# Optimization experiments

Hardware: AMD Instinct MI355X
Metric: run time of the kernel (lower is better)

Reference implementation:

```python
import jax, jax.numpy as jnp
import numpy as np

N_NODES = 50000
N_EDGES = 1600000
IN_DIM = 128
HID = 64
EPS = 1e-6


def setup_inputs() -> dict:
    key = jax.random.key(0)
    ks = jax.random.split(key, 12)
    def g(k, shape, scale):
        return jax.random.normal(k, shape, dtype=jnp.float32) * scale
    x = g(ks[0], (N_NODES, IN_DIM), 1.0)
    edge_index = jax.random.randint(ks[1], (2, N_EDGES), 0, N_NODES, dtype=jnp.int64)
    return {
        "x": x,
        "edge_index": edge_index,
        "w0s": g(ks[2], (IN_DIM, HID), 1.0 / np.sqrt(IN_DIM)),
        "w0n": g(ks[3], (IN_DIM, HID), 1.0 / np.sqrt(IN_DIM)),
        "w1s": g(ks[4], (HID, HID), 1.0 / np.sqrt(HID)),
        "w1n": g(ks[5], (HID, HID), 1.0 / np.sqrt(HID)),
        "w2s": g(ks[6], (HID, HID), 1.0 / np.sqrt(HID)),
        "w2n": g(ks[7], (HID, HID), 1.0 / np.sqrt(HID)),
        "mw1": g(ks[8], (HID, 32), 1.0 / np.sqrt(HID)),
        "mb1": jnp.zeros((32,), jnp.float32),
        "mw2": g(ks[9], (32, 1), 1.0 / np.sqrt(32.0)),
        "mb2": jnp.zeros((1,), jnp.float32),
    }


def _uhg_layer(h, src, dst, inv_deg, ws, wn):
    # transform-then-gather (cheaper: GEMM at node granularity, gather at edge granularity)
    msg = (h @ wn)[src]                                    # [E, HID]
    agg = jax.ops.segment_sum(msg, dst, num_segments=N_NODES) * inv_deg  # mean over in-neighbors
    h2 = jax.nn.relu(h @ ws + agg)
    # projective (UHG) normalization: map embedding back onto the unit sphere / projective rep
    return h2 / (jnp.linalg.norm(h2, axis=-1, keepdims=True) + EPS)


def reference(x, edge_index, w0s, w0n, w1s, w1n, w2s, w2n, mw1, mb1, mw2, mb2):
    src, dst = edge_index[0], edge_index[1]
    deg = jax.ops.segment_sum(jnp.ones((N_EDGES,), jnp.float32), dst, num_segments=N_NODES)
    inv_deg = (1.0 / jnp.maximum(deg, 1.0))[:, None]       # [N,1]
    h = _uhg_layer(x, src, dst, inv_deg, w0s, w0n)
    h = _uhg_layer(h, src, dst, inv_deg, w1s, w1n)
    h = _uhg_layer(h, src, dst, inv_deg, w2s, w2n)
    h = jax.nn.relu(h @ mw1 + mb1)                         # [N,32]
    return jax.nn.sigmoid(h @ mw2 + mb2)                   # [N,1]
```

## Files before the change

kernel.cpp:

```cpp
#include <hip/hip_runtime.h>
#include <hip/hip_bf16.h>
#include <math.h>

#define N_NODES 50000
#define N_EDGES 1600000
#define IN_DIM  128
#define HID     64
#define EPB     4096
#define NBLK    391
#define NB      391
#define CAP     8192
static constexpr float EPS = 1e-6f;

typedef __attribute__((ext_vector_type(8))) short          short8;
typedef __attribute__((ext_vector_type(8))) unsigned short ushort8;
typedef __attribute__((ext_vector_type(4))) unsigned short bf16x4_t;
typedef __attribute__((ext_vector_type(4))) int            i32x4;
typedef __attribute__((ext_vector_type(4))) float          f32x4;
typedef __attribute__((ext_vector_type(2))) float          f32x2;

__device__ __forceinline__ float bf2f(unsigned int hi_bits) {
    union { unsigned int i; float f; } c; c.i = hi_bits; return c.f;
}
__device__ __forceinline__ unsigned short f2bf(float f) {
    union { float f; unsigned int i; } c; c.f = f;
    unsigned int r = c.i + 0x7FFFu + ((c.i >> 16) & 1u);
    return (unsigned short)(r >> 16);
}
__device__ __forceinline__ unsigned char f2fp8(float f) {
    int p = __builtin_amdgcn_cvt_pk_fp8_f32(f, f, 0, false);
    return (unsigned char)(p & 0xff);
}


template <int K>
__device__ __forceinline__ void pack_body(const float* __restrict__ wS,
                                          const float* __restrict__ wN,
                                          unsigned short* __restrict__ pS,
                                          unsigned short* __restrict__ pN, int blk) {
    constexpr int NSLOT = (K / 32) * 4 * 64;
    int slot = blk * 256 + (int)threadIdx.x;
    if (slot >= NSLOT) return;
    int lane = slot & 63;
    int ct   = slot >> 6;
    int t    = ct & 3;
    int c    = ct >> 2;
    int m    = lane & 15;
    int quad = lane >> 4;
    int col  = t * 16 + m;
#pragma unroll
    for (int j = 0; j < 8; ++j) {
        int k = c * 32 + quad * 8 + j;
        pS[slot * 8 + j] = f2bf(wS[k * 64 + col]);
        pN[slot * 8 + j] = f2bf(wN[k * 64 + col]);
    }
}


__global__ __launch_bounds__(256) void bucket_count_pack(
    const int* __restrict__ ei, int* __restrict__ blockCounts,
    const float* __restrict__ w0s, const float* __restrict__ w0n,
    const float* __restrict__ w1s, const float* __restrict__ w1n,
    const float* __restrict__ w2s, const float* __restrict__ w2n,
    unsigned short* __restrict__ p0S, unsigned short* __restrict__ p0N,
    unsigned short* __restrict__ p1S, unsigned short* __restrict__ p1N,
    unsigned short* __restrict__ p2S, unsigned short* __restrict__ p2N,
    unsigned char* __restrict__ hnq) {
    if (blockIdx.x >= NBLK) {
        int blk = blockIdx.x - NBLK;
        if (blk == 7 && threadIdx.x >= 128 && threadIdx.x < 144)
            ((unsigned int*)(hnq + (size_t)N_NODES * HID))[threadIdx.x - 128] = 0u;
        if (blk < 4)      pack_body<IN_DIM>(w0s, w0n, p0S, p0N, blk);
        else if (blk < 6) pack_body<HID>(w1s, w1n, p1S, p1N, blk - 4);
        else              pack_body<HID>(w2s, w2n, p2S, p2N, blk - 6);
        return;
    }
    __shared__ int hist[NB];
    for (int i = threadIdx.x; i < NB; i += 256) hist[i] = 0;
    __syncthreads();
    int base = blockIdx.x * EPB;
    int lim  = min(EPB, N_EDGES - base);
    for (int i = threadIdx.x; i < lim; i += 256)
        atomicAdd(&hist[ei[N_EDGES + base + i] >> 7], 1);
    __syncthreads();
    for (int b = threadIdx.x; b < NB; b += 256)
        blockCounts[blockIdx.x * NB + b] = hist[b];
}

template <int K, bool F32IN>
__device__ __forceinline__ void gemm_body(
    const void* __restrict__ Av,
    const unsigned short* __restrict__ pS,
    const unsigned short* __restrict__ pN,
    float* __restrict__ hs, unsigned char* __restrict__ hnq, int blk) {
    constexpr int NC = K / 32;
    int lane = threadIdx.x & 63;
    int wv   = threadIdx.x >> 6;
    int tile = blk * 4 + wv;
    if (tile >= N_NODES / 16) return;
    int m    = lane & 15;
    int quad = lane >> 4;

    const short8* pSf = (const short8*)pS;
    const short8* pNf = (const short8*)pN;

    f32x4 accS[4], accN[4];
#pragma unroll
    for (int t = 0; t < 4; ++t) {
        accS[t] = (f32x4){0.f, 0.f, 0.f, 0.f};
        accN[t] = (f32x4){0.f, 0.f, 0.f, 0.f};
    }
#pragma unroll
    for (int c = 0; c < NC; ++c) {
        short8 a;
        if constexpr (F32IN) {
            const float* Af = (const float*)Av + ((size_t)tile * 16 + m) * K + quad * 8 + c * 32;
            f32x4 a0 = *(const f32x4*)Af;
            f32x4 a1 = *(const f32x4*)(Af + 4);
#pragma unroll
            for (int k = 0; k < 4; ++k) a[k]     = (short)f2bf(a0[k]);
#pragma unroll
            for (int k = 0; k < 4; ++k) a[k + 4] = (short)f2bf(a1[k]);
        } else {
            const short8* Af = (const short8*)((const unsigned short*)Av +
                               ((size_t)tile * 16 + m) * K + quad * 8);
            a = Af[c * 4];
        }
#pragma unroll
        for (int t = 0; t < 4; ++t) {
            short8 bs = pSf[(c * 4 + t) * 64 + lane];
            short8 bn = pNf[(c * 4 + t) * 64 + lane];
            accS[t] = __builtin_amdgcn_mfma_f32_16x16x32_bf16(a, bs, accS[t], 0, 0, 0);
            accN[t] = __builtin_amdgcn_mfma_f32_16x16x32_bf16(a, bn, accN[t], 0, 0, 0);
        }
    }
    int row0 = tile * 16 + quad * 4;
#pragma unroll
    for (int t = 0; t < 4; ++t) {
#pragma unroll
        for (int r = 0; r < 4; ++r) {
            size_t o = (size_t)(row0 + r) * HID + t * 16 + m;
            hs[o]  = accS[t][r];
            hnq[o] = f2fp8(accN[t][r]);
        }
    }
}

__global__ __launch_bounds__(256) void col_sum_gemm0(
    const int* __restrict__ blockCounts, int* __restrict__ totals,
    const float* __restrict__ x,
    const unsigned short* __restrict__ p0S, const unsigned short* __restrict__ p0N,
    float* __restrict__ hs, unsigned char* __restrict__ hnq) {
    if (blockIdx.x >= NB) {
        gemm_body<IN_DIM, true>(x, p0S, p0N, hs, hnq, blockIdx.x - NB);
        return;
    }
    __shared__ int ws[4];
    int b = blockIdx.x;
    int s = 0;
    for (int i = threadIdx.x; i < NBLK; i += 256) s += blockCounts[i * NB + b];
#pragma unroll
    for (int off = 32; off >= 1; off >>= 1) s += __shfl_xor(s, off, 64);
    if ((threadIdx.x & 63) == 0) ws[threadIdx.x >> 6] = s;
    __syncthreads();
    if (threadIdx.x == 0) totals[b] = ws[0] + ws[1] + ws[2] + ws[3];
}

__global__ __launch_bounds__(256) void col_fix_base(int* __restrict__ blockCounts,
                                                    const int* __restrict__ totals,
                                                    int* __restrict__ bucketBase) {
    __shared__ int vals[NBLK];
    __shared__ int sbase;
    int b = blockIdx.x;
    for (int i = threadIdx.x; i < NBLK; i += 256) vals[i] = blockCounts[i * NB + b];
    if (threadIdx.x < 64) {
        int lane = threadIdx.x;
        int s = 0;
        for (int i = lane; i < b; i += 64) s += totals[i];
#pragma unroll
        for (int off = 32; off >= 1; off >>= 1) s += __shfl_xor(s, off, 64);
        if (lane == 0) {
            sbase = s;
            bucketBase[b] = s;
            if (b == NB - 1) bucketBase[NB] = s + totals[b];
        }
    }
    __syncthreads();
    if (threadIdx.x < 64) {
        int lane  = threadIdx.x;
        int carry = sbase;
        for (int base = 0; base < NBLK; base += 64) {
            int i = base + lane;
            int v = (i < NBLK) ? vals[i] : 0;
            int incl = v;
#pragma unroll
            for (int off = 1; off < 64; off <<= 1) {
                int t = __shfl_up(incl, off, 64);
                if (lane >= off) incl += t;
            }
            if (i < NBLK) vals[i] = carry + incl - v;
            carry += __shfl(incl, 63, 64);
        }
    }
    __syncthreads();
    for (int i = threadIdx.x; i < NBLK; i += 256) blockCounts[i * NB + b] = vals[i];
}

__global__ __launch_bounds__(256) void bucket_scatter(const int* __restrict__ ei,
                                                      const int* __restrict__ blockCounts,
                                                      unsigned int* __restrict__ bucketPacked) {
    __shared__ int cur[NB];
    for (int b = threadIdx.x; b < NB; b += 256)
        cur[b] = blockCounts[blockIdx.x * NB + b];
    __syncthreads();
    int base = blockIdx.x * EPB;
    int lim  = min(EPB, N_EDGES - base);
    for (int i = threadIdx.x; i < lim; i += 256) {
        int s = ei[base + i];
        int d = ei[N_EDGES + base + i];
        int pos = atomicAdd(&cur[d >> 7], 1);
        bucketPacked[pos] = ((unsigned int)s << 7) | (unsigned int)(d & 127);
    }
}

__global__ __launch_bounds__(256) void node_scan_scatter(
    const unsigned int* __restrict__ bucketPacked, const int* __restrict__ bucketBase,
    int* __restrict__ rowptr, int* __restrict__ csr_src) {
    __shared__ int cnt[128];
    __shared__ int half0;
    __shared__ unsigned int stage[CAP];
    int tid = threadIdx.x;
    if (tid < 128) cnt[tid] = 0;
    __syncthreads();
    int beg = bucketBase[blockIdx.x], end = bucketBase[blockIdx.x + 1];
    int n = end - beg;
    for (int i = tid; i < n; i += 256) {
        unsigned int e = bucketPacked[beg + i];
        if (i < CAP) stage[i] = e;
        atomicAdd(&cnt[e & 127], 1);
    }
    __syncthreads();
    int lane = tid & 63;
    int v    = (tid < 128) ? cnt[tid] : 0;
    int incl = v;
#pragma unroll
    for (int off = 1; off < 64; off <<= 1) {
        int t = __shfl_up(incl, off, 64);
        if (lane >= off) incl += t;
    }
    if (tid == 63) half0 = incl;
    __syncthreads();
    int base  = beg + ((tid >= 64 && tid < 128) ? half0 : 0);
    int start = base + incl - v;
    int node  = blockIdx.x * 128 + tid;
    if (tid < 128) {
        if (node < N_NODES) rowptr[node] = start;
        cnt[tid] = start;
    }
    if (blockIdx.x == 0 && tid == 128) rowptr[N_NODES] = N_EDGES;
    __syncthreads();
    for (int i = tid; i < n; i += 256) {
        unsigned int e = (i < CAP) ? stage[i] : bucketPacked[beg + i];
        int pos = atomicAdd(&cnt[e & 127], 1);
        csr_src[pos] = (int)(e >> 7);
    }
}

template <int K, bool F32IN>
__global__ __launch_bounds__(256) void gemm_dual_mfma(
    const void* __restrict__ Av,
    const unsigned short* __restrict__ pS,
    const unsigned short* __restrict__ pN,
    float* __restrict__ hs, unsigned char* __restrict__ hnq) {
    gemm_body<K, F32IN>(Av, pS, pN, hs, hnq, blockIdx.x);
}

template <bool MLP>
__global__ __launch_bounds__(256) void agg_update(
    const int* __restrict__ rowptr, const int* __restrict__ csr_src,
    const unsigned char* __restrict__ hnq, const float* __restrict__ hs,
    unsigned short* __restrict__ hb_out,
    const float* __restrict__ mw1, const float* __restrict__ mb1,
    const float* __restrict__ mw2, const float* __restrict__ mb2,
    float* __restrict__ out) {
    __shared__ float sW1[MLP ? HID * 32 : 1];
    __shared__ float sW2[MLP ? 32 : 1];
    __shared__ float sB1[MLP ? 32 : 1];
    __shared__ float sH[MLP ? 16 * 68 : 1];
    if (MLP) {
        for (int i = threadIdx.x; i < HID * 32; i += 256) sW1[i] = mw1[i];
        if (threadIdx.x < 32) { sW2[threadIdx.x] = mw2[threadIdx.x]; sB1[threadIdx.x] = mb1[threadIdx.x]; }
        __syncthreads();
    }
    int sn   = threadIdx.x >> 4;
    int r    = threadIdx.x & 15;
    int node = blockIdx.x * 16 + sn;
    int beg = rowptr[node];
    int end = rowptr[node + 1];
    int deg = end - beg;
    int tbase = beg & ~7;
    int nbat  = (end - tbase + 7) >> 3;
    const i32x4* ip = (const i32x4*)(csr_src + tbase);
    const unsigned char* hrow = hnq + r * 4;

    f32x2 acc2[2];
    acc2[0] = (f32x2){0.f, 0.f};
    acc2[1] = (f32x2){0.f, 0.f};
    int pr = tbase - beg;

#pragma unroll 2
    for (int t = 0; t < nbat; ++t) {
        i32x4 a = ip[2 * t];
        i32x4 b = ip[2 * t + 1];
        int p0 = pr + 8 * t;
        int si[8];
#pragma unroll
        for (int u = 0; u < 4; ++u) {
            si[u]     = ((unsigned)(p0 + u)     < (unsigned)deg) ? a[u] : N_NODES;
            si[u + 4] = ((unsigned)(p0 + 4 + u) < (unsigned)deg) ? b[u] : N_NODES;
        }
        unsigned wv[8];
#pragma unroll
        for (int u = 0; u < 8; ++u)
            wv[u] = *(const unsigned*)(hrow + ((unsigned)si[u] << 6));
#pragma unroll
        for (int u = 0; u < 8; ++u) {
#if __has_builtin(__builtin_amdgcn_cvt_pk_f32_fp8)
            acc2[0] += __builtin_amdgcn_cvt_pk_f32_fp8((int)wv[u], false);
            acc2[1] += __builtin_amdgcn_cvt_pk_f32_fp8((int)wv[u], true);
#else
            acc2[0] += (f32x2){__builtin_amdgcn_cvt_f32_fp8((int)wv[u], 0),
                               __builtin_amdgcn_cvt_f32_fp8((int)wv[u], 1)};
            acc2[1] += (f32x2){__builtin_amdgcn_cvt_f32_fp8((int)wv[u], 2),
                               __builtin_amdgcn_cvt_f32_fp8((int)wv[u], 3)};
#endif
        }
    }

    float acc[4] = {acc2[0][0], acc2[0][1], acc2[1][0], acc2[1][1]};
    float invdeg = 1.0f / fmaxf((float)deg, 1.0f);
    f32x4 h = *(const f32x4*)(hs + (size_t)node * HID + r * 4);
    float v[4], ss = 0.f;
#pragma unroll
    for (int k = 0; k < 4; ++k) {
        v[k] = fmaxf(fmaf(acc[k], invdeg, h[k]), 0.f);
        ss += v[k] * v[k];
    }
    ss += __shfl_xor(ss, 1, 64);
    ss += __shfl_xor(ss, 2, 64);
    ss += __shfl_xor(ss, 4, 64);
    ss += __shfl_xor(ss, 8, 64);
    float rs = 1.0f / (sqrtf(ss) + EPS);
    if (MLP) {
#pragma unroll
        for (int k = 0; k < 4; ++k) sH[sn * 68 + r * 4 + k] = v[k] * rs;
        __syncthreads();
        int c0 = r * 2;
        float y0 = sB1[c0], y1 = sB1[c0 + 1];
        const float* hrow2 = &sH[sn * 68];
#pragma unroll 8
        for (int k = 0; k < HID; ++k) {
            float hv = hrow2[k];
            y0 = fmaf(hv, sW1[k * 32 + c0], y0);
            y1 = fmaf(hv, sW1[k * 32 + c0 + 1], y1);
        }
        float p = fmaxf(y0, 0.f) * sW2[c0] + fmaxf(y1, 0.f) * sW2[c0 + 1];
        p += __shfl_xor(p, 1, 64);
        p += __shfl_xor(p, 2, 64);
        p += __shfl_xor(p, 4, 64);
        p += __shfl_xor(p, 8, 64);
        if (r == 0) out[node] = 1.0f / (1.0f + __expf(-(p + mb2[0])));
    } else {
        bf16x4_t o;
#pragma unroll
        for (int k = 0; k < 4; ++k) o[k] = f2bf(v[k] * rs);
        *(bf16x4_t*)(hb_out + (size_t)node * HID + r * 4) = o;
    }
}

extern "C" void kernel_launch(void* const* d_in, const int* in_sizes, int n_in,
                              void* d_out, int out_size, void* d_ws, size_t ws_size,
                              hipStream_t stream) {
    const float* x   = (const float*)d_in[0];
    const int*   ei  = (const int*)d_in[1];
    const float* w0s = (const float*)d_in[2];
    const float* w0n = (const float*)d_in[3];
    const float* w1s = (const float*)d_in[4];
    const float* w1n = (const float*)d_in[5];
    const float* w2s = (const float*)d_in[6];
    const float* w2n = (const float*)d_in[7];
    const float* mw1 = (const float*)d_in[8];
    const float* mb1 = (const float*)d_in[9];
    const float* mw2 = (const float*)d_in[10];
    const float* mb2 = (const float*)d_in[11];
    float*       out = (float*)d_out;

    int* rowptr      = (int*)d_ws;
    int* csr_src     = rowptr + 50432;
    int* blockCounts = csr_src + N_EDGES;
    int* bucketBase  = blockCounts + 153600;
    int* totals      = bucketBase + 512;
    unsigned int* bucketPacked = (unsigned int*)(totals + 512);
    const size_t NH = (size_t)N_NODES * HID;
    float*          hs  = (float*)(bucketPacked + N_EDGES);
    unsigned char*  hnq = (unsigned char*)(hs + NH);
    unsigned short* hb  = (unsigned short*)(hnq + NH + 64);
    unsigned short* p0S = hb + NH;
    unsigned short* p0N = p0S + IN_DIM * HID;
    unsigned short* p1S = p0N + IN_DIM * HID;
    unsigned short* p1N = p1S + HID * HID;
    unsigned short* p2S = p1N + HID * HID;
    unsigned short* p2N = p2S + HID * HID;

    const int nodeGrid = N_NODES / 16;
    const int gemmGrid = (N_NODES / 16 + 3) / 4;

    bucket_count_pack<<<NBLK + 8, 256, 0, stream>>>(
        ei, blockCounts, w0s, w0n, w1s, w1n, w2s, w2n,
        p0S, p0N, p1S, p1N, p2S, p2N, hnq);
    col_sum_gemm0<<<NB + gemmGrid, 256, 0, stream>>>(
        blockCounts, totals, x, p0S, p0N, hs, hnq);
    col_fix_base<<<NB, 256, 0, stream>>>(blockCounts, totals, bucketBase);
    bucket_scatter<<<NBLK, 256, 0, stream>>>(ei, blockCounts, bucketPacked);
    node_scan_scatter<<<NB, 256, 0, stream>>>(bucketPacked, bucketBase, rowptr, csr_src);

    agg_update<false><<<nodeGrid, 256, 0, stream>>>(
        rowptr, csr_src, hnq, hs, hb, nullptr, nullptr, nullptr, nullptr, nullptr);

    gemm_dual_mfma<HID, false><<<gemmGrid, 256, 0, stream>>>(hb, p1S, p1N, hs, hnq);
    agg_update<false><<<nodeGrid, 256, 0, stream>>>(
        rowptr, csr_src, hnq, hs, hb, nullptr, nullptr, nullptr, nullptr, nullptr);

    gemm_dual_mfma<HID, false><<<gemmGrid, 256, 0, stream>>>(hb, p2S, p2N, hs, hnq);
    agg_update<true><<<nodeGrid, 256, 0, stream>>>(
        rowptr, csr_src, hnq, hs, nullptr, mw1, mb1, mw2, mb2, out);
}
```

Before: 223.6 us.

## Fuse next-layer GEMM into aggregation and pad CSR rows to multiples of eight

Each non-final aggregation kernel now stages its normalized 16-node tile in shared memory as bf16 and runs the next layer's dual MFMA GEMM directly, writing the fp32 self term and fp8 neighbor term into ping-pong buffers. This removes the two standalone GEMM launches and the bf16 hidden-state round trip through global memory. The CSR is also rebuilt with per-node padding to multiples of eight using a dummy node index, so the gather loop can drop its per-edge bounds masking. The cost is a larger padded CSR buffer, per-bucket capacity assumptions (8192 slots), and an extra block barrier plus MFMA work inside the latency-bound gather kernel.

```diff
diff --git a/kernel.cpp b/kernel.cpp
--- a/kernel.cpp
+++ b/kernel.cpp
@@ -10,6 +10,7 @@
 #define NBLK    391
 #define NB      391
 #define CAP     8192
+#define PBKT    8192
 static constexpr float EPS = 1e-6f;
 
 typedef __attribute__((ext_vector_type(8))) short          short8;
@@ -19,9 +20,6 @@
 typedef __attribute__((ext_vector_type(4))) float          f32x4;
 typedef __attribute__((ext_vector_type(2))) float          f32x2;
 
-__device__ __forceinline__ float bf2f(unsigned int hi_bits) {
-    union { unsigned int i; float f; } c; c.i = hi_bits; return c.f;
-}
 __device__ __forceinline__ unsigned short f2bf(float f) {
     union { float f; unsigned int i; } c; c.f = f;
     unsigned int r = c.i + 0x7FFFu + ((c.i >> 16) & 1u);
@@ -65,11 +63,15 @@
     unsigned short* __restrict__ p0S, unsigned short* __restrict__ p0N,
     unsigned short* __restrict__ p1S, unsigned short* __restrict__ p1N,
     unsigned short* __restrict__ p2S, unsigned short* __restrict__ p2N,
-    unsigned char* __restrict__ hnq) {
+    unsigned char* __restrict__ hnqA, unsigned char* __restrict__ hnqB) {
     if (blockIdx.x >= NBLK) {
         int blk = blockIdx.x - NBLK;
-        if (blk == 7 && threadIdx.x >= 128 && threadIdx.x < 144)
-            ((unsigned int*)(hnq + (size_t)N_NODES * HID))[threadIdx.x - 128] = 0u;
+        if (blk == 7) {
+            if (threadIdx.x >= 128 && threadIdx.x < 144)
+                ((unsigned int*)(hnqA + (size_t)N_NODES * HID))[threadIdx.x - 128] = 0u;
+            if (threadIdx.x >= 144 && threadIdx.x < 160)
+                ((unsigned int*)(hnqB + (size_t)N_NODES * HID))[threadIdx.x - 144] = 0u;
+        }
         if (blk < 4)      pack_body<IN_DIM>(w0s, w0n, p0S, p0N, blk);
         else if (blk < 6) pack_body<HID>(w1s, w1n, p1S, p1N, blk - 4);
         else              pack_body<HID>(w2s, w2n, p2S, p2N, blk - 6);
@@ -223,9 +225,9 @@
     }
 }
 
-__global__ __launch_bounds__(256) void node_scan_scatter(
+__global__ __launch_bounds__(256) void node_scan_scatter_pad(
     const unsigned int* __restrict__ bucketPacked, const int* __restrict__ bucketBase,
-    int* __restrict__ rowptr, int* __restrict__ csr_src) {
+    int* __restrict__ pbeg, int* __restrict__ rdeg, int* __restrict__ csr_pad) {
     __shared__ int cnt[128];
     __shared__ int half0;
     __shared__ unsigned int stage[CAP];
@@ -242,7 +244,8 @@
     __syncthreads();
     int lane = tid & 63;
     int v    = (tid < 128) ? cnt[tid] : 0;
-    int incl = v;
+    int vp   = (v + 7) & ~7;
+    int incl = vp;
 #pragma unroll
     for (int off = 1; off < 64; off <<= 1) {
         int t = __shfl_up(incl, off, 64);
@@ -250,39 +253,33 @@
     }
     if (tid == 63) half0 = incl;
     __syncthreads();
-    int base  = beg + ((tid >= 64 && tid < 128) ? half0 : 0);
-    int start = base + incl - v;
+    int start = blockIdx.x * PBKT + ((tid >= 64 && tid < 128) ? half0 : 0) + incl - vp;
     int node  = blockIdx.x * 128 + tid;
-    if (tid < 128) {
-        if (node < N_NODES) rowptr[node] = start;
+    if (tid < 128 && node < N_NODES) {
+        pbeg[node] = start;
+        rdeg[node] = v;
+        for (int j = v; j < vp; ++j) csr_pad[start + j] = N_NODES;
         cnt[tid] = start;
     }
-    if (blockIdx.x == 0 && tid == 128) rowptr[N_NODES] = N_EDGES;
     __syncthreads();
     for (int i = tid; i < n; i += 256) {
         unsigned int e = (i < CAP) ? stage[i] : bucketPacked[beg + i];
         int pos = atomicAdd(&cnt[e & 127], 1);
-        csr_src[pos] = (int)(e >> 7);
-    }
-}
-
-template <int K, bool F32IN>
-__global__ __launch_bounds__(256) void gemm_dual_mfma(
-    const void* __restrict__ Av,
-    const unsigned short* __restrict__ pS,
-    const unsigned short* __restrict__ pN,
-    float* __restrict__ hs, unsigned char* __restrict__ hnq) {
-    gemm_body<K, F32IN>(Av, pS, pN, hs, hnq, blockIdx.x);
+        csr_pad[pos] = (int)(e >> 7);
+    }
 }
 
 template <bool MLP>
 __global__ __launch_bounds__(256) void agg_update(
-    const int* __restrict__ rowptr, const int* __restrict__ csr_src,
+    const int* __restrict__ pbeg, const int* __restrict__ rdeg,
+    const int* __restrict__ csr_pad,
     const unsigned char* __restrict__ hnq, const float* __restrict__ hs,
-    unsigned short* __restrict__ hb_out,
+    const unsigned short* __restrict__ pS, const unsigned short* __restrict__ pN,
+    float* __restrict__ hs2, unsigned char* __restrict__ hnq2,
     const float* __restrict__ mw1, const float* __restrict__ mb1,
     const float* __restrict__ mw2, const float* __restrict__ mb2,
     float* __restrict__ out) {
+    __shared__ unsigned short sA[MLP ? 1 : 16 * 80];
     __shared__ float sW1[MLP ? HID * 32 : 1];
     __shared__ float sW2[MLP ? 32 : 1];
     __shared__ float sB1[MLP ? 32 : 1];
@@ -295,34 +292,27 @@
     int sn   = threadIdx.x >> 4;
     int r    = threadIdx.x & 15;
     int node = blockIdx.x * 16 + sn;
-    int beg = rowptr[node];
-    int end = rowptr[node + 1];
-    int deg = end - beg;
-    int tbase = beg & ~7;
-    int nbat  = (end - tbase + 7) >> 3;
-    const i32x4* ip = (const i32x4*)(csr_src + tbase);
-    const unsigned char* hrow = hnq + r * 4;
+    int beg  = pbeg[node];
+    int dg   = rdeg[node];
+    int nbat = (dg + 7) >> 3;
+    const i32x4* ip = (const i32x4*)(csr_pad + beg);
+    unsigned r4 = (unsigned)(r * 4);
 
     f32x2 acc2[2];
     acc2[0] = (f32x2){0.f, 0.f};
     acc2[1] = (f32x2){0.f, 0.f};
-    int pr = tbase - beg;
 
 #pragma unroll 2
     for (int t = 0; t < nbat; ++t) {
         i32x4 a = ip[2 * t];
         i32x4 b = ip[2 * t + 1];
-        int p0 = pr + 8 * t;
-        int si[8];
-#pragma unroll
-        for (int u = 0; u < 4; ++u) {
-            si[u]     = ((unsigned)(p0 + u)     < (unsigned)deg) ? a[u] : N_NODES;
-            si[u + 4] = ((unsigned)(p0 + 4 + u) < (unsigned)deg) ? b[u] : N_NODES;
-        }
         unsigned wv[8];
 #pragma unroll
-        for (int u = 0; u < 8; ++u)
-            wv[u] = *(const unsigned*)(hrow + ((unsigned)si[u] << 6));
+        for (int u = 0; u < 4; ++u)
+            wv[u]     = *(const unsigned*)(hnq + (((unsigned)a[u] << 6) + r4));
+#pragma unroll
+        for (int u = 0; u < 4; ++u)
+            wv[u + 4] = *(const unsigned*)(hnq + (((unsigned)b[u] << 6) + r4));
 #pragma unroll
         for (int u = 0; u < 8; ++u) {
 #if __has_builtin(__builtin_amdgcn_cvt_pk_f32_fp8)
@@ -338,7 +328,7 @@
     }
 
     float acc[4] = {acc2[0][0], acc2[0][1], acc2[1][0], acc2[1][1]};
-    float invdeg = 1.0f / fmaxf((float)deg, 1.0f);
+    float invdeg = 1.0f / fmaxf((float)dg, 1.0f);
     f32x4 h = *(const f32x4*)(hs + (size_t)node * HID + r * 4);
     float v[4], ss = 0.f;
 #pragma unroll
@@ -351,7 +341,42 @@
     ss += __shfl_xor(ss, 4, 64);
     ss += __shfl_xor(ss, 8, 64);
     float rs = 1.0f / (sqrtf(ss) + EPS);
-    if (MLP) {
+
+    if constexpr (!MLP) {
+        unsigned short* ap = &sA[sn * 80 + r * 4];
+#pragma unroll
+        for (int k = 0; k < 4; ++k) ap[k] = f2bf(v[k] * rs);
+        __syncthreads();
+        int lane = threadIdx.x & 63;
+        int wv_  = threadIdx.x >> 6;
+        int m    = lane & 15;
+        int quad = lane >> 4;
+        const short8* pB = (const short8*)((wv_ < 2) ? pS : pN);
+        int t0 = (wv_ & 1) * 2;
+        f32x4 gacc[2];
+        gacc[0] = (f32x4){0.f, 0.f, 0.f, 0.f};
+        gacc[1] = (f32x4){0.f, 0.f, 0.f, 0.f};
+#pragma unroll
+        for (int c = 0; c < 2; ++c) {
+            short8 a = *(const short8*)&sA[m * 80 + quad * 8 + c * 32];
+#pragma unroll
+            for (int tt = 0; tt < 2; ++tt) {
+                short8 b = pB[(c * 4 + t0 + tt) * 64 + lane];
+                gacc[tt] = __builtin_amdgcn_mfma_f32_16x16x32_bf16(a, b, gacc[tt], 0, 0, 0);
+            }
+        }
+        int row0 = blockIdx.x * 16 + quad * 4;
+#pragma unroll
+        for (int tt = 0; tt < 2; ++tt) {
+            int col = (t0 + tt) * 16 + m;
+#pragma unroll
+            for (int rr = 0; rr < 4; ++rr) {
+                size_t o = (size_t)(row0 + rr) * HID + col;
+                if (wv_ < 2) hs2[o]  = gacc[tt][rr];
+                else         hnq2[o] = f2fp8(gacc[tt][rr]);
+            }
+        }
+    } else {
 #pragma unroll
         for (int k = 0; k < 4; ++k) sH[sn * 68 + r * 4 + k] = v[k] * rs;
         __syncthreads();
@@ -370,11 +395,6 @@
         p += __shfl_xor(p, 4, 64);
         p += __shfl_xor(p, 8, 64);
         if (r == 0) out[node] = 1.0f / (1.0f + __expf(-(p + mb2[0])));
-    } else {
-        bf16x4_t o;
-#pragma unroll
-        for (int k = 0; k < 4; ++k) o[k] = f2bf(v[k] * rs);
-        *(bf16x4_t*)(hb_out + (size_t)node * HID + r * 4) = o;
     }
 }
 
@@ -395,17 +415,19 @@
     const float* mb2 = (const float*)d_in[11];
     float*       out = (float*)d_out;
 
-    int* rowptr      = (int*)d_ws;
-    int* csr_src     = rowptr + 50432;
-    int* blockCounts = csr_src + N_EDGES;
+    int* pbeg        = (int*)d_ws;
+    int* rdeg        = pbeg + 50048;
+    int* blockCounts = rdeg + 50048;
     int* bucketBase  = blockCounts + 153600;
     int* totals      = bucketBase + 512;
     unsigned int* bucketPacked = (unsigned int*)(totals + 512);
+    int* csr_pad     = (int*)(bucketPacked + N_EDGES);
     const size_t NH = (size_t)N_NODES * HID;
-    float*          hs  = (float*)(bucketPacked + N_EDGES);
-    unsigned char*  hnq = (unsigned char*)(hs + NH);
-    unsigned short* hb  = (unsigned short*)(hnq + NH + 64);
-    unsigned short* p0S = hb + NH;
+    float*          hsA  = (float*)(csr_pad + NB * PBKT);
+    unsigned char*  hnqA = (unsigned char*)(hsA + NH);
+    float*          hsB  = (float*)(hnqA + NH + 64);
+    unsigned char*  hnqB = (unsigned char*)(hsB + NH);
+    unsigned short* p0S = (unsigned short*)(hnqB + NH + 64);
     unsigned short* p0N = p0S + IN_DIM * HID;
     unsigned short* p1S = p0N + IN_DIM * HID;
     unsigned short* p1N = p1S + HID * HID;
@@ -417,21 +439,23 @@
 
     bucket_count_pack<<<NBLK + 8, 256, 0, stream>>>(
         ei, blockCounts, w0s, w0n, w1s, w1n, w2s, w2n,
-        p0S, p0N, p1S, p1N, p2S, p2N, hnq);
+        p0S, p0N, p1S, p1N, p2S, p2N, hnqA, hnqB);
     col_sum_gemm0<<<NB + gemmGrid, 256, 0, stream>>>(
-        blockCounts, totals, x, p0S, p0N, hs, hnq);
+        blockCounts, totals, x, p0S, p0N, hsA, hnqA);
     col_fix_base<<<NB, 256, 0, stream>>>(blockCounts, totals, bucketBase);
     bucket_scatter<<<NBLK, 256, 0, stream>>>(ei, blockCounts, bucketPacked);
-    node_scan_scatter<<<NB, 256, 0, stream>>>(bucketPacked, bucketBase, rowptr, csr_src);
+    node_scan_scatter_pad<<<NB, 256, 0, stream>>>(bucketPacked, bucketBase,
+                                                  pbeg, rdeg, csr_pad);
 
     agg_update<false><<<nodeGrid, 256, 0, stream>>>(
-        rowptr, csr_src, hnq, hs, hb, nullptr, nullptr, nullptr, nullptr, nullptr);
-
-    gemm_dual_mfma<HID, false><<<gemmGrid, 256, 0, stream>>>(hb, p1S, p1N, hs, hnq);
+        pbeg, rdeg, csr_pad, hnqA, hsA, p1S, p1N, hsB, hnqB,
+        nullptr, nullptr, nullptr, nullptr, nullptr);
+
     agg_update<false><<<nodeGrid, 256, 0, stream>>>(
-        rowptr, csr_src, hnq, hs, hb, nullptr, nullptr, nullptr, nullptr, nullptr);
-
-    gemm_dual_mfma<HID, false><<<gemmGrid, 256, 0, stream>>>(hb, p2S, p2N, hs, hnq);
+        pbeg, rdeg, csr_pad, hnqB, hsB, p2S, p2N, hsA, hnqA,
+        nullptr, nullptr, nullptr, nullptr, nullptr);
+
     agg_update<true><<<nodeGrid, 256, 0, stream>>>(
-        rowptr, csr_src, hnq, hs, nullptr, mw1, mb1, mw2, mb2, out);
-}
+        pbeg, rdeg, csr_pad, hnqA, hsA, nullptr, nullptr, nullptr, nullptr,
+        mw1, mb1, mw2, mb2, out);
+}
```

Result: faster. 204.1 us (-8.7%).
